# Kernel tuning notes

Hardware: AMD Instinct MI355X
Metric: run time of the kernel (lower is better)

Reference implementation:

```python
import jax, jax.numpy as jnp
import numpy as np

D_MODEL = 1024
NUM_HEADS = 16
HEAD_DIM = D_MODEL // NUM_HEADS


def setup_inputs() -> dict:
    key = jax.random.key(0)
    ks = jax.random.split(key, 11)
    B, S = 2, 2048
    s = 1.0 / np.sqrt(D_MODEL)
    inp = {
        "query": jax.random.normal(ks[0], (B, S, D_MODEL), jnp.float32),
        "key": jax.random.normal(ks[1], (B, S, D_MODEL), jnp.float32),
        "value": jax.random.normal(ks[2], (B, S, D_MODEL), jnp.float32),
        "Wq": jax.random.normal(ks[3], (D_MODEL, D_MODEL), jnp.float32) * s,
        "bq": jnp.zeros((D_MODEL,), jnp.float32),
        "Wk": jax.random.normal(ks[4], (D_MODEL, D_MODEL), jnp.float32) * s,
        "bk": jnp.zeros((D_MODEL,), jnp.float32),
        "Wv": jax.random.normal(ks[5], (D_MODEL, D_MODEL), jnp.float32) * s,
        "bv": jnp.zeros((D_MODEL,), jnp.float32),
        "Wo": jax.random.normal(ks[6], (D_MODEL, D_MODEL), jnp.float32) * s,
        "bo": jnp.zeros((D_MODEL,), jnp.float32),
    }
    return inp


def _split_heads(x):
    B, S, _ = x.shape
    return x.reshape(B, S, NUM_HEADS, HEAD_DIM).transpose(0, 2, 1, 3)  # [B,H,S,d]


def reference(query, key, value, Wq, bq, Wk, bk, Wv, bv, Wo, bo):
    Q = _split_heads(query @ Wq.T + bq)
    K = _split_heads(key @ Wk.T + bk)
    V = _split_heads(value @ Wv.T + bv)
    scale = 1.0 / jnp.sqrt(jnp.asarray(HEAD_DIM, jnp.float32))
    scores = jnp.einsum("bhqd,bhkd->bhqk", Q, K) * scale  # [B,H,S,S]
    weights = jax.nn.softmax(scores, axis=-1)
    attn = jnp.einsum("bhqk,bhkd->bhqd", weights, V)
    B, H, S, d = attn.shape
    attn = attn.transpose(0, 2, 1, 3).reshape(B, S, H * d)
    return attn @ Wo.T + bo
```

## Files before the change

### kernel.cpp

```cpp
#include <hip/hip_runtime.h>
#include <hip/hip_bf16.h>


typedef unsigned short u16;
typedef __attribute__((ext_vector_type(8))) short short8;
typedef __attribute__((ext_vector_type(4))) float floatx4;

__device__ __forceinline__ float bf2f(u16 x) {
  return __uint_as_float(((unsigned)x) << 16);
}
__device__ __forceinline__ u16 f2bf(float f) {
  unsigned x = __float_as_uint(f);
  return (u16)((x + 0x7fffu + ((x >> 16) & 1u)) >> 16);
}
__device__ __forceinline__ ushort2 pk_bf16(float a, float b) {
  __hip_bfloat162 h2 = __float22bfloat162_rn(make_float2(a, b));
  ushort2 u;
  __builtin_memcpy(&u, &h2, 4);
  return u;
}
__device__ __forceinline__ short8 cvt8(float4 a, float4 b) {
  const ushort2 p0 = pk_bf16(a.x, a.y), p1 = pk_bf16(a.z, a.w);
  const ushort2 p2 = pk_bf16(b.x, b.y), p3 = pk_bf16(b.z, b.w);
  union { short8 s8; ushort us[8]; } u;
  u.us[0] = p0.x; u.us[1] = p0.y; u.us[2] = p1.x; u.us[3] = p1.y;
  u.us[4] = p2.x; u.us[5] = p2.y; u.us[6] = p3.x; u.us[7] = p3.y;
  return u.s8;
}
#if __has_builtin(__builtin_amdgcn_exp2f)
#define EXP2(x) __builtin_amdgcn_exp2f(x)
#else
#define EXP2(x) exp2f(x)
#endif
__device__ __forceinline__ void gll16(const u16* g, u16* lds) {
  __builtin_amdgcn_global_load_lds((const __attribute__((address_space(1))) void*)g,
                                   (__attribute__((address_space(3))) void*)lds,
                                   16, 0, 0);
}

__global__ __launch_bounds__(256) void cvt_kernel(
    const float* __restrict__ wq, const float* __restrict__ wk,
    const float* __restrict__ wv, const float* __restrict__ wo,
    const float* __restrict__ bq, const float* __restrict__ bk,
    const float* __restrict__ bv, const float* __restrict__ bo,
    u16* __restrict__ ws) {
  const int i4 = (blockIdx.x * 256 + threadIdx.x) * 4;
  const float* src;
  u16* dst;
  int local;
  if (i4 < 1048576)       { src = wq; dst = ws + 12582912; local = i4; }
  else if (i4 < 2097152)  { src = wk; dst = ws + 13631488; local = i4 - 1048576; }
  else if (i4 < 3145728)  { src = wv; dst = ws + 14680064; local = i4 - 2097152; }
  else if (i4 < 4194304)  { src = wo; dst = ws + 15728640; local = i4 - 3145728; }
  else if (i4 < 4195328)  { src = bq; dst = ws + 16777216; local = i4 - 4194304; }
  else if (i4 < 4196352)  { src = bk; dst = ws + 16779264; local = i4 - 4195328; }
  else if (i4 < 4197376)  { src = bv; dst = ws + 16781312; local = i4 - 4196352; }
  else                    { src = bo; dst = ws + 16783360; local = i4 - 4197376; }
  const float4 f = *(const float4*)(src + local);
  ushort4 o;
  o.x = f2bf(f.x); o.y = f2bf(f.y); o.z = f2bf(f.z); o.w = f2bf(f.w);
  *(ushort4*)(dst + local) = o;
}

template <int MTILE, bool XF32>
__device__ __forceinline__ void gemm_tile(
    const u16* __restrict__ X16, const float* __restrict__ X32,
    const u16* __restrict__ W, const u16* __restrict__ bias,
    u16* __restrict__ out16, float* __restrict__ out32,
    int row0, int col0, int mode, float oscale, u16* As, u16* Bs) {
  constexpr int NI = MTILE / 32;
  constexpr int ABUF = MTILE * 32;
  const int tid = threadIdx.x;
  const int w = tid >> 6, l = tid & 63;
  const int lan = l & 15, quad = l >> 4;
  const int wm = w & 1, wn = w >> 1;

  floatx4 acc[NI][4];
#pragma unroll
  for (int i = 0; i < NI; ++i)
#pragma unroll
    for (int j = 0; j < 4; ++j) acc[i][j] = (floatx4)0.0f;

  const int r0 = tid >> 2, kq0 = tid & 3;
  const int r1 = (tid + 256) >> 2;
  const int woff = w * 512;
  const u16* Xa0 = XF32 ? nullptr : X16 + (size_t)(row0 + r0) * 1024 + kq0 * 8;
  const float* Xf0 = XF32 ? X32 + (size_t)(row0 + r0) * 1024 + kq0 * 8 : nullptr;
  const float* Xf1 = XF32 ? X32 + (size_t)(row0 + r1) * 1024 + kq0 * 8 : nullptr;
  const u16* Wb0 = W + (size_t)(col0 + r0) * 1024 + kq0 * 8;
  const u16* Wb1 = W + (size_t)(col0 + r1) * 1024 + kq0 * 8;

#define STAGEW(buf, kt)                                          \
  do {                                                           \
    gll16(Wb0 + (kt) * 32, Bs + (buf) * 4096 + woff);            \
    gll16(Wb1 + (kt) * 32, Bs + (buf) * 4096 + 2048 + woff);     \
  } while (0)
#define STAGEXG(buf, kt)                                         \
  do {                                                           \
    gll16(Xa0 + (kt) * 32, As + (buf) * ABUF + woff);            \
  } while (0)

  float4 xl0a, xl0b, xl1a, xl1b;
  if (XF32) {
    xl0a = *(const float4*)(Xf0 + 0);
    xl0b = *(const float4*)(Xf0 + 4);
    xl1a = *(const float4*)(Xf1 + 0);
    xl1b = *(const float4*)(Xf1 + 4);
    STAGEW(0, 0);
    *(short8*)(As + tid * 8) = cvt8(xl0a, xl0b);
    *(short8*)(As + 2048 + tid * 8) = cvt8(xl1a, xl1b);
  } else {
    STAGEXG(0, 0);
    STAGEW(0, 0);
  }
  int cur = 0;
  for (int kt = 0; kt < 32; ++kt) {
    const int nb = cur == 2 ? 0 : cur + 1;
    if (kt < 31) {
      if (XF32) {
        xl0a = *(const float4*)(Xf0 + (kt + 1) * 32);
        xl0b = *(const float4*)(Xf0 + (kt + 1) * 32 + 4);
        xl1a = *(const float4*)(Xf1 + (kt + 1) * 32);
        xl1b = *(const float4*)(Xf1 + (kt + 1) * 32 + 4);
        STAGEW(nb, kt + 1);
        __asm__ volatile("s_waitcnt vmcnt(6) lgkmcnt(0)" ::: "memory");
      } else {
        STAGEXG(nb, kt + 1);
        STAGEW(nb, kt + 1);
        __asm__ volatile("s_waitcnt vmcnt(3)" ::: "memory");
      }
    } else {
      if (XF32)
        __asm__ volatile("s_waitcnt vmcnt(0) lgkmcnt(0)" ::: "memory");
      else
        __asm__ volatile("s_waitcnt vmcnt(0)" ::: "memory");
    }
    __builtin_amdgcn_s_barrier();

    const u16* Ab = As + cur * ABUF;
    const u16* Bb = Bs + cur * 4096;
    short8 af[NI], bfr[4];
#pragma unroll
    for (int i = 0; i < NI; ++i)
      af[i] = *(const short8*)(Ab + (wm * (MTILE / 2) + i * 16 + lan) * 32 + quad * 8);
#pragma unroll
    for (int j = 0; j < 4; ++j)
      bfr[j] = *(const short8*)(Bb + (wn * 64 + j * 16 + lan) * 32 + quad * 8);
#pragma unroll
    for (int i = 0; i < NI; ++i)
#pragma unroll
      for (int j = 0; j < 4; ++j)
        acc[i][j] = __builtin_amdgcn_mfma_f32_16x16x32_bf16(af[i], bfr[j], acc[i][j], 0, 0, 0);

    if (XF32 && kt < 31) {
      *(short8*)(As + nb * ABUF + tid * 8) = cvt8(xl0a, xl0b);
      *(short8*)(As + nb * ABUF + 2048 + tid * 8) = cvt8(xl1a, xl1b);
    }
    cur = nb;
  }
#undef STAGEW
#undef STAGEXG

#pragma unroll
  for (int i = 0; i < NI; ++i) {
    const int mb = row0 + wm * (MTILE / 2) + i * 16 + quad * 4;
#pragma unroll
    for (int j = 0; j < 4; ++j) {
      const int n = col0 + wn * 64 + j * 16 + lan;
      const float bv = bf2f(bias[n]);
      if (mode == 0) {
#pragma unroll
        for (int r = 0; r < 4; ++r)
          out16[(size_t)(mb + r) * 1024 + n] = f2bf((acc[i][j][r] + bv) * oscale);
      } else if (mode == 1) {
        const int b = mb >> 11;
        const int h = n >> 6, dd = n & 63;
        u16* base = out16 + (size_t)((b * 16 + h) * 64 + dd) * 2048;
        const int s0 = mb & 2047;
        const int k0 = s0 & 63;
        const int sp0 = (s0 & ~63) | (((k0 >> 5) & 1) << 5) | (((k0 >> 2) & 3) << 3) |
                        (((k0 >> 4) & 1) << 2);
        ushort4 ov;
        ov.x = f2bf(acc[i][j][0] + bv);
        ov.y = f2bf(acc[i][j][1] + bv);
        ov.z = f2bf(acc[i][j][2] + bv);
        ov.w = f2bf(acc[i][j][3] + bv);
        *(ushort4*)(base + sp0) = ov;
      } else {
#pragma unroll
        for (int r = 0; r < 4; ++r)
          out32[(size_t)(mb + r) * 1024 + n] = acc[i][j][r] + bv;
      }
    }
  }
}

__global__ __launch_bounds__(256) void qkv_kernel(
    const float* __restrict__ xq, const float* __restrict__ xk,
    const float* __restrict__ xv,
    const u16* __restrict__ Wq, const u16* __restrict__ Wk, const u16* __restrict__ Wv,
    const u16* __restrict__ bq, const u16* __restrict__ bk, const u16* __restrict__ bv,
    u16* __restrict__ Qo, u16* __restrict__ Ko, u16* __restrict__ Vto) {
  __shared__ __align__(16) u16 As[3 * 4096];
  __shared__ __align__(16) u16 Bs[3 * 4096];
  const int bx = blockIdx.x;
  const int xcd = bx & 7;
  const int j = bx >> 3;
  const int c = j & 7;
  const int gidx = j >> 3;
  const int g = gidx * 8 + xcd;
  const int which = g >> 5;
  const int tile_m = g & 31;
  const int col0 = c * 128;
  const float* X = which == 0 ? xq : (which == 1 ? xk : xv);
  const u16* W = which == 0 ? Wq : (which == 1 ? Wk : Wv);
  const u16* bias = which == 0 ? bq : (which == 1 ? bk : bv);
  u16* out = which == 0 ? Qo : (which == 1 ? Ko : Vto);
  const float C = 0.125f * 1.4426950408889634f;
  gemm_tile<128, true>(nullptr, X, W, bias, out, nullptr, tile_m * 128, col0,
                       which == 2 ? 1 : 0, which == 0 ? C : 1.0f, As, Bs);
}

__global__ __launch_bounds__(256) void proj_kernel(
    const u16* __restrict__ X, const u16* __restrict__ W,
    const u16* __restrict__ bias, float* __restrict__ out) {
  __shared__ __align__(16) u16 As[3 * 2048];
  __shared__ __align__(16) u16 Bs[3 * 4096];
  const int bx = blockIdx.x;
  const int xcd = bx & 7;
  const int j = bx >> 3;
  const int c = j & 7;
  const int gidx = j >> 3;
  const int tm = xcd * 8 + gidx;
  gemm_tile<64, false>(X, nullptr, W, bias, nullptr, out, tm * 64, c * 128, 2,
                       1.0f, As, Bs);
}

#define FIXMAX 16.0f
#define KPAD 72
__global__ __launch_bounds__(256, 2) void attn_kernel(
    const u16* __restrict__ Q, const u16* __restrict__ K,
    const u16* __restrict__ Vt, u16* __restrict__ O) {
  __shared__ __align__(16) u16 KV[4][64 * KPAD];
  const int tid = threadIdx.x;
  const int w = tid >> 6, l = tid & 63;
  const int lan = l & 15, quad = l >> 4;
  const int g = w >> 1;
  const int h2 = w & 1;
  const int id = blockIdx.x + (blockIdx.y << 4);
  const int xcd = id & 7;
  const int jj = id >> 3;
  const int bh = xcd * 4 + (jj >> 4);
  const int q0 = (jj & 15) * 128;
  const int b = bh >> 4, h = bh & 15;
  const u16* Qg = Q + (size_t)(b * 2048 + q0) * 1024 + h * 64;
  const u16* Kg = K + (size_t)(b * 2048) * 1024 + h * 64;
  const u16* Vg = Vt + (size_t)((b * 16 + h) * 64) * 2048;

  short8 qf[4][2];
#pragma unroll
  for (int mi = 0; mi < 4; ++mi)
#pragma unroll
    for (int kk = 0; kk < 2; ++kk)
      qf[mi][kk] = *(const short8*)(Qg + (size_t)(g * 64 + mi * 16 + lan) * 1024 +
                                    kk * 32 + quad * 8);

  float lrun[4] = {0.f, 0.f, 0.f, 0.f};
  floatx4 oacc[4][4];
#pragma unroll
  for (int mi = 0; mi < 4; ++mi)
#pragma unroll
    for (int nd = 0; nd < 4; ++nd) oacc[mi][nd] = (floatx4)0.0f;

  const int rowA = tid >> 3, colq = (tid & 7) * 8;
  const int rowB = rowA + 32;

  short8 k0 = *(const short8*)(Kg + (size_t)rowA * 1024 + colq);
  short8 k1 = *(const short8*)(Kg + (size_t)rowB * 1024 + colq);
  short8 v0 = *(const short8*)(Vg + (size_t)rowA * 2048 + colq);
  short8 v1 = *(const short8*)(Vg + (size_t)rowB * 2048 + colq);
  *(short8*)(KV[0] + rowA * KPAD + colq) = k0;
  *(short8*)(KV[0] + rowB * KPAD + colq) = k1;
  *(short8*)(KV[2] + rowA * KPAD + colq) = v0;
  *(short8*)(KV[2] + rowB * KPAD + colq) = v1;
  __syncthreads();

  for (int kt = 0; kt < 32; ++kt) {
    const int cur = kt & 1;
    if (kt < 31) {
      const int kn = kt + 1;
      k0 = *(const short8*)(Kg + (size_t)(kn * 64 + rowA) * 1024 + colq);
      k1 = *(const short8*)(Kg + (size_t)(kn * 64 + rowB) * 1024 + colq);
      v0 = *(const short8*)(Vg + (size_t)rowA * 2048 + kn * 64 + colq);
      v1 = *(const short8*)(Vg + (size_t)rowB * 2048 + kn * 64 + colq);
    }
    const u16* Kc = KV[cur];
    const u16* Vc = KV[2 + cur];

    floatx4 sacc[4][2];
#pragma unroll
    for (int mi = 0; mi < 4; ++mi)
#pragma unroll
      for (int nj2 = 0; nj2 < 2; ++nj2) sacc[mi][nj2] = (floatx4)(-FIXMAX);
#pragma unroll
    for (int kk = 0; kk < 2; ++kk) {
      short8 kf[2];
#pragma unroll
      for (int nj2 = 0; nj2 < 2; ++nj2)
        kf[nj2] = *(const short8*)(Kc + ((2 * h2 + nj2) * 16 + lan) * KPAD +
                                   kk * 32 + quad * 8);
      __builtin_amdgcn_s_setprio(1);
#pragma unroll
      for (int mi = 0; mi < 4; ++mi)
#pragma unroll
        for (int nj2 = 0; nj2 < 2; ++nj2)
          sacc[mi][nj2] = __builtin_amdgcn_mfma_f32_16x16x32_bf16(
              kf[nj2], qf[mi][kk], sacc[mi][nj2], 0, 0, 0);
      __builtin_amdgcn_s_setprio(0);
    }

    short8 vf[4];
#pragma unroll
    for (int nd = 0; nd < 4; ++nd)
      vf[nd] = *(const short8*)(Vc + (nd * 16 + lan) * KPAD + h2 * 32 + quad * 8);

    short8 pb[4];
#pragma unroll
    for (int mi = 0; mi < 4; ++mi) {
      float p[2][4];
#pragma unroll
      for (int nj2 = 0; nj2 < 2; ++nj2)
#pragma unroll
        for (int r = 0; r < 4; ++r) p[nj2][r] = EXP2(sacc[mi][nj2][r]);
      float s0 = 0.f, s1 = 0.f;
#pragma unroll
      for (int r = 0; r < 4; ++r) {
        s0 += p[0][r];
        s1 += p[1][r];
      }
      lrun[mi] += s0 + s1;
      const ushort2 w0 = pk_bf16(p[0][0], p[0][1]);
      const ushort2 w1 = pk_bf16(p[0][2], p[0][3]);
      const ushort2 w2 = pk_bf16(p[1][0], p[1][1]);
      const ushort2 w3 = pk_bf16(p[1][2], p[1][3]);
      union { short8 s8; ushort us[8]; } u;
      u.us[0] = w0.x; u.us[1] = w0.y; u.us[2] = w1.x; u.us[3] = w1.y;
      u.us[4] = w2.x; u.us[5] = w2.y; u.us[6] = w3.x; u.us[7] = w3.y;
      pb[mi] = u.s8;
    }

    __builtin_amdgcn_s_setprio(1);
#pragma unroll
    for (int mi = 0; mi < 4; ++mi)
#pragma unroll
      for (int nd = 0; nd < 4; ++nd)
        oacc[mi][nd] = __builtin_amdgcn_mfma_f32_16x16x32_bf16(
            vf[nd], pb[mi], oacc[mi][nd], 0, 0, 0);
    __builtin_amdgcn_s_setprio(0);

    if (kt < 31) {
      const int nxt = cur ^ 1;
      *(short8*)(KV[nxt] + rowA * KPAD + colq) = k0;
      *(short8*)(KV[nxt] + rowB * KPAD + colq) = k1;
      *(short8*)(KV[2 + nxt] + rowA * KPAD + colq) = v0;
      *(short8*)(KV[2 + nxt] + rowB * KPAD + colq) = v1;
      __syncthreads();
    }
  }

#pragma unroll
  for (int mi = 0; mi < 4; ++mi) {
    lrun[mi] += __shfl_xor(lrun[mi], 16);
    lrun[mi] += __shfl_xor(lrun[mi], 32);
  }
  __syncthreads();
  float4* obuf = (float4*)&KV[0][0];
  float* lbuf = (float*)&KV[0][0] + 8192;
  if (h2 == 1) {
#pragma unroll
    for (int mi = 0; mi < 4; ++mi) {
#pragma unroll
      for (int nd = 0; nd < 4; ++nd) {
        const int fi = mi * 4 + nd;
        float4 t;
        t.x = oacc[mi][nd][0]; t.y = oacc[mi][nd][1];
        t.z = oacc[mi][nd][2]; t.w = oacc[mi][nd][3];
        obuf[(g * 64 + l) * 16 + ((fi + l) & 15)] = t;
      }
      lbuf[(g * 64 + l) * 4 + mi] = lrun[mi];
    }
  }
  __syncthreads();
  if (h2 == 0) {
#pragma unroll
    for (int mi = 0; mi < 4; ++mi) {
      const float lt = lrun[mi] + lbuf[(g * 64 + l) * 4 + mi];
      const float inv = 1.0f / lt;
      const int qg = b * 2048 + q0 + g * 64 + mi * 16 + lan;
#pragma unroll
      for (int nd = 0; nd < 4; ++nd) {
        const int fi = mi * 4 + nd;
        const float4 t = obuf[(g * 64 + l) * 16 + ((fi + l) & 15)];
        ushort4 ov;
        ov.x = f2bf((oacc[mi][nd][0] + t.x) * inv);
        ov.y = f2bf((oacc[mi][nd][1] + t.y) * inv);
        ov.z = f2bf((oacc[mi][nd][2] + t.z) * inv);
        ov.w = f2bf((oacc[mi][nd][3] + t.w) * inv);
        *(ushort4*)(O + (size_t)qg * 1024 + h * 64 + nd * 16 + quad * 4) = ov;
      }
    }
  }
}

extern "C" void kernel_launch(void* const* d_in, const int* in_sizes, int n_in,
                              void* d_out, int out_size, void* d_ws, size_t ws_size,
                              hipStream_t stream) {
  const float* query = (const float*)d_in[0];
  const float* key_ = (const float*)d_in[1];
  const float* value = (const float*)d_in[2];
  const float* Wq = (const float*)d_in[3];
  const float* bq = (const float*)d_in[4];
  const float* Wk = (const float*)d_in[5];
  const float* bk = (const float*)d_in[6];
  const float* Wv = (const float*)d_in[7];
  const float* bv = (const float*)d_in[8];
  const float* Wo = (const float*)d_in[9];
  const float* bo = (const float*)d_in[10];
  float* out = (float*)d_out;

  u16* ws = (u16*)d_ws;
  u16* cWq = ws + 12582912;
  u16* cWk = ws + 13631488;
  u16* cWv = ws + 14680064;
  u16* cWo = ws + 15728640;
  u16* cbq = ws + 16777216;
  u16* cbk = ws + 16779264;
  u16* cbv = ws + 16781312;
  u16* cbo = ws + 16783360;
  u16* Qw = ws + 17301504;
  u16* Kw = ws + 21495808;
  u16* Vtw = ws + 25690112;
  u16* Ow = ws + 29884416;

  cvt_kernel<<<4100, 256, 0, stream>>>(Wq, Wk, Wv, Wo, bq, bk, bv, bo, ws);
  qkv_kernel<<<768, 256, 0, stream>>>(query, key_, value, cWq, cWk, cWv,
                                      cbq, cbk, cbv, Qw, Kw, Vtw);
  attn_kernel<<<dim3(16, 32), 256, 0, stream>>>(Qw, Kw, Vtw, Ow);
  proj_kernel<<<512, 256, 0, stream>>>(Ow, cWo, cbo, out);
}
```

Before: 225.2 us.

## Prefetch fp32 activations two k-tiles ahead with double-buffered registers

In the fp32-input GEMM path, X loads are now issued two iterations ahead into alternating register sets (xa/xb). The bf16 conversion and LDS write happen before the barrier for the next buffer instead of after the MFMAs, so global load latency has a full iteration to hide. This costs extra VGPRs for the second register set, which may reduce occupancy, and the vmcnt counts must match the number of outstanding loads.

After: 242.7 us. 1.08x slower.

```diff
diff --git a/kernel.cpp b/kernel.cpp
--- a/kernel.cpp
+++ b/kernel.cpp
@@ -99,16 +99,26 @@
   do {                                                           \
     gll16(Xa0 + (kt) * 32, As + (buf) * ABUF + woff);            \
   } while (0)
-
-  float4 xl0a, xl0b, xl1a, xl1b;
-  if (XF32) {
-    xl0a = *(const float4*)(Xf0 + 0);
-    xl0b = *(const float4*)(Xf0 + 4);
-    xl1a = *(const float4*)(Xf1 + 0);
-    xl1b = *(const float4*)(Xf1 + 4);
+#define LOADX(s, kt)                                             \
+  do {                                                           \
+    s##0 = *(const float4*)(Xf0 + (kt) * 32);                    \
+    s##1 = *(const float4*)(Xf0 + (kt) * 32 + 4);                \
+    s##2 = *(const float4*)(Xf1 + (kt) * 32);                    \
+    s##3 = *(const float4*)(Xf1 + (kt) * 32 + 4);                \
+  } while (0)
+#define CVTWR(s, buf)                                            \
+  do {                                                           \
+    *(short8*)(As + (buf) * ABUF + tid * 8) = cvt8(s##0, s##1);  \
+    *(short8*)(As + (buf) * ABUF + 2048 + tid * 8) = cvt8(s##2, s##3); \
+  } while (0)
+
+  float4 xa0, xa1, xa2, xa3, xb0, xb1, xb2, xb3;
+  if constexpr (XF32) {
+    LOADX(xa, 0);
     STAGEW(0, 0);
-    *(short8*)(As + tid * 8) = cvt8(xl0a, xl0b);
-    *(short8*)(As + 2048 + tid * 8) = cvt8(xl1a, xl1b);
+    LOADX(xb, 1);
+    __asm__ volatile("s_waitcnt vmcnt(6)" ::: "memory");
+    CVTWR(xa, 0);
   } else {
     STAGEXG(0, 0);
     STAGEW(0, 0);
@@ -116,24 +126,30 @@
   int cur = 0;
   for (int kt = 0; kt < 32; ++kt) {
     const int nb = cur == 2 ? 0 : cur + 1;
-    if (kt < 31) {
-      if (XF32) {
-        xl0a = *(const float4*)(Xf0 + (kt + 1) * 32);
-        xl0b = *(const float4*)(Xf0 + (kt + 1) * 32 + 4);
-        xl1a = *(const float4*)(Xf1 + (kt + 1) * 32);
-        xl1b = *(const float4*)(Xf1 + (kt + 1) * 32 + 4);
+    if constexpr (XF32) {
+      if (kt <= 30) {
         STAGEW(nb, kt + 1);
-        __asm__ volatile("s_waitcnt vmcnt(6) lgkmcnt(0)" ::: "memory");
+        if (kt <= 29) {
+          if ((kt & 1) == 0) LOADX(xa, kt + 2);
+          else               LOADX(xb, kt + 2);
+          __asm__ volatile("s_waitcnt vmcnt(6)" ::: "memory");
+        } else {
+          __asm__ volatile("s_waitcnt vmcnt(2)" ::: "memory");
+        }
+        if ((kt & 1) == 0) CVTWR(xb, nb);
+        else               CVTWR(xa, nb);
+        __asm__ volatile("s_waitcnt lgkmcnt(0)" ::: "memory");
       } else {
+        __asm__ volatile("s_waitcnt vmcnt(0) lgkmcnt(0)" ::: "memory");
+      }
+    } else {
+      if (kt < 31) {
         STAGEXG(nb, kt + 1);
         STAGEW(nb, kt + 1);
         __asm__ volatile("s_waitcnt vmcnt(3)" ::: "memory");
-      }
-    } else {
-      if (XF32)
-        __asm__ volatile("s_waitcnt vmcnt(0) lgkmcnt(0)" ::: "memory");
-      else
+      } else {
         __asm__ volatile("s_waitcnt vmcnt(0)" ::: "memory");
+      }
     }
     __builtin_amdgcn_s_barrier();
 
@@ -151,15 +167,12 @@
 #pragma unroll
       for (int j = 0; j < 4; ++j)
         acc[i][j] = __builtin_amdgcn_mfma_f32_16x16x32_bf16(af[i], bfr[j], acc[i][j], 0, 0, 0);
-
-    if (XF32 && kt < 31) {
-      *(short8*)(As + nb * ABUF + tid * 8) = cvt8(xl0a, xl0b);
-      *(short8*)(As + nb * ABUF + 2048 + tid * 8) = cvt8(xl1a, xl1b);
-    }
     cur = nb;
   }
 #undef STAGEW
 #undef STAGEXG
+#undef LOADX
+#undef CVTWR
 
 #pragma unroll
   for (int i = 0; i < NI; ++i) {
```
